# Performance work log

Measured on AMD Instinct MI355X. Metric: run time of the kernel, lower is better.

## Reference

```python
import jax, jax.numpy as jnp
import numpy as np

B, T, D, H = 512, 512, 128, 64


def _lstm(x, Wih, Whh, b):
    """Single-layer batch-first LSTM, PyTorch gate order (i, f, g, o).
    x: [B, T, Din]; Wih: [4Hc, Din]; Whh: [4Hc, Hc]; b: [4Hc] (= b_ih + b_hh).
    Returns (outputs [B, T, Hc], final_hidden [B, Hc]).
    """
    Hc = Whh.shape[1]
    Bn = x.shape[0]
    # Precompute input projections for all timesteps: [B, T, 4Hc]
    xp = jnp.einsum('bti,gi->btg', x, Wih) + b

    def step(carry, xt):
        h, c = carry
        g = xt + h @ Whh.T                      # [B, 4Hc]
        i = jax.nn.sigmoid(g[:, :Hc])
        f = jax.nn.sigmoid(g[:, Hc:2 * Hc])
        gg = jnp.tanh(g[:, 2 * Hc:3 * Hc])
        o = jax.nn.sigmoid(g[:, 3 * Hc:])
        c = f * c + i * gg
        h = o * jnp.tanh(c)
        return (h, c), h

    init = (jnp.zeros((Bn, Hc), x.dtype), jnp.zeros((Bn, Hc), x.dtype))
    (h_last, _), ys = jax.lax.scan(step, init, jnp.swapaxes(xp, 0, 1))
    return jnp.swapaxes(ys, 0, 1), h_last


def setup_inputs() -> dict:
    key = jax.random.key(0)
    ks = jax.random.split(key, 7)
    se = 1.0 / np.sqrt(H)   # PyTorch LSTM init scale (encoder, hidden=H)
    sd = 1.0 / np.sqrt(D)   # decoder, hidden=D
    return {
        'x': jax.random.normal(ks[0], (B, T, D), jnp.float32),
        'Wih_e': jax.random.uniform(ks[1], (4 * H, D), jnp.float32, -se, se),
        'Whh_e': jax.random.uniform(ks[2], (4 * H, H), jnp.float32, -se, se),
        'b_e': jax.random.uniform(ks[3], (4 * H,), jnp.float32, -se, se),
        'Wih_d': jax.random.uniform(ks[4], (4 * D, H), jnp.float32, -sd, sd),
        'Whh_d': jax.random.uniform(ks[5], (4 * D, D), jnp.float32, -sd, sd),
        'b_d': jax.random.uniform(ks[6], (4 * D,), jnp.float32, -sd, sd),
    }


def reference(x, Wih_e, Whh_e, b_e, Wih_d, Whh_d, b_d):
    # Encoder: take final hidden state [B, H]
    _, h = _lstm(x, Wih_e, Whh_e, b_e)
    # hidden.repeat(T,1,1).permute(1,0,2) -> tile across time: [B, T, H]
    hrep = jnp.broadcast_to(h[:, None, :], (h.shape[0], x.shape[1], h.shape[1]))
    # Decoder: full output sequence [B, T, D]
    reconstructed, _ = _lstm(hrep, Wih_d, Whh_d, b_d)
    return reconstructed
```

## Files before the change

kernel.cpp:

```cpp
#include <hip/hip_runtime.h>

#define TT 512

typedef float f32x4 __attribute__((ext_vector_type(4)));

template<int CTRL>
__device__ __forceinline__ float dpp_mov(float v) {
    return __int_as_float(__builtin_amdgcn_mov_dpp(__float_as_int(v), CTRL, 0xF, 0xF, true));
}
__device__ __forceinline__ float swz_xor4(float v) {
    return __int_as_float(__builtin_amdgcn_ds_swizzle(__float_as_int(v), 0x101F));
}

#define LOG2E 1.4426950408889634f
#define NEG2LOG2E -2.8853900817779268f

__device__ __forceinline__ float merge8(float* s) {
    s[0] += dpp_mov<0xB1>(s[4]);
    s[1] += dpp_mov<0xB1>(s[5]);
    s[2] += dpp_mov<0xB1>(s[6]);
    s[3] += dpp_mov<0xB1>(s[7]);
    s[0] += dpp_mov<0x4E>(s[2]);
    s[1] += dpp_mov<0x4E>(s[3]);
    return s[0] + swz_xor4(s[1]);
}

__global__ __launch_bounds__(1024, 4)
void dec_kernel(const float* __restrict__ h_enc,
                const float* __restrict__ Wih,
                const float* __restrict__ Whh,
                const float* __restrict__ bias,
                float* __restrict__ out)
{
    const int tid = threadIdx.x;
    const int gg  = tid >> 3;
    const int q   = tid & 7;
    const int q0 = q & 1, q1 = (q >> 1) & 1, q2 = (q >> 2) & 1;
    const int msk2 = (q0 << 1) | q1;
    const int b0  = blockIdx.x * 2;

    __shared__ __align__(16) float he[2][64];
    __shared__ __align__(16) float hb[2][2 * 160];

    if (tid < 128) he[tid >> 6][tid & 63] = h_enc[(size_t)(b0 + (tid >> 6)) * 64 + (tid & 63)];
    if (tid < 256) {
        int r = tid >> 7, j = tid & 127;
        hb[0][r * 160 + j + 4 * (j >> 4)] = 0.f;
    }

    f32x4 w[4][4];
    #pragma unroll
    for (int m = 0; m < 4; ++m) {
        const float* src = Whh + (size_t)((m ^ msk2) * 128 + gg) * 128 + 16 * q;
        #pragma unroll
        for (int c = 0; c < 4; ++c) w[m][c] = *(const f32x4*)(src + 4 * c);
    }

    const int t4own = 2 * q0 + q1;
    const float sA = (t4own == 2) ? 2.f : 1.f;
    const float sC = (t4own == 2) ? -1.f : 0.f;
    const float nsA = -LOG2E * sA;
    const bool writer = (q0 == 0) && (q1 == 0);
    const int rr  = q2;
    const int oA  = q2 * 160;
    const int oB  = (q2 ^ 1) * 160;
    const int kres = 20 * q;
    const int pwj = q2 * 160 + gg + 4 * (gg >> 4);

    __syncthreads();

    float xp;
    {
        const float* heA = he[q2] + 8 * q;
        const float* heB = he[q2 ^ 1] + 8 * q;
        f32x4 hA0 = *(const f32x4*)heA, hA1 = *(const f32x4*)(heA + 4);
        f32x4 hB0 = *(const f32x4*)heB, hB1 = *(const f32x4*)(heB + 4);
        float s[8];
        #pragma unroll
        for (int m = 0; m < 4; ++m) {
            const float* ws = Wih + (size_t)((m ^ msk2) * 128 + gg) * 64 + 8 * q;
            f32x4 w0 = *(const f32x4*)ws, w1 = *(const f32x4*)(ws + 4);
            float aA = 0.f, aB = 0.f;
            aA = fmaf(w0.x, hA0.x, aA); aA = fmaf(w0.y, hA0.y, aA);
            aA = fmaf(w0.z, hA0.z, aA); aA = fmaf(w0.w, hA0.w, aA);
            aA = fmaf(w1.x, hA1.x, aA); aA = fmaf(w1.y, hA1.y, aA);
            aA = fmaf(w1.z, hA1.z, aA); aA = fmaf(w1.w, hA1.w, aA);
            aB = fmaf(w0.x, hB0.x, aB); aB = fmaf(w0.y, hB0.y, aB);
            aB = fmaf(w0.z, hB0.z, aB); aB = fmaf(w0.w, hB0.w, aB);
            aB = fmaf(w1.x, hB1.x, aB); aB = fmaf(w1.y, hB1.y, aB);
            aB = fmaf(w1.z, hB1.z, aB); aB = fmaf(w1.w, hB1.w, aB);
            s[2 * m]     = aA;
            s[2 * m + 1] = aB;
        }
        xp = merge8(s) + bias[t4own * 128 + gg];
    }

    float c_state = 0.f;
    size_t optr = ((size_t)(b0 + rr) * TT) * 128 + gg;

#define DSTEP(CUR, NXT) {                                                      \
    const float* bAp = (CUR) + oA + kres;                                      \
    const float* bBp = (CUR) + oB + kres;                                      \
    f32x4 ch[4]; float s[8];                                                   \
    _Pragma("unroll") for (int c = 0; c < 4; ++c) ch[c] = *(const f32x4*)(bAp + 4 * c); \
    _Pragma("unroll") for (int m = 0; m < 4; ++m) { float a = 0.f;             \
        _Pragma("unroll") for (int c = 0; c < 4; ++c) {                        \
            a = fmaf(w[m][c].x, ch[c].x, a); a = fmaf(w[m][c].y, ch[c].y, a);  \
            a = fmaf(w[m][c].z, ch[c].z, a); a = fmaf(w[m][c].w, ch[c].w, a); }\
        s[2 * m] = a; }                                                        \
    _Pragma("unroll") for (int c = 0; c < 4; ++c) ch[c] = *(const f32x4*)(bBp + 4 * c); \
    _Pragma("unroll") for (int m = 0; m < 4; ++m) { float a = 0.f;             \
        _Pragma("unroll") for (int c = 0; c < 4; ++c) {                        \
            a = fmaf(w[m][c].x, ch[c].x, a); a = fmaf(w[m][c].y, ch[c].y, a);  \
            a = fmaf(w[m][c].z, ch[c].z, a); a = fmaf(w[m][c].w, ch[c].w, a); }\
        s[2 * m + 1] = a; }                                                    \
    float z = merge8(s) + xp;                                                  \
    float ez = __builtin_amdgcn_exp2f(z * nsA);                                \
    float v  = fmaf(__builtin_amdgcn_rcpf(1.0f + ez), sA, sC);                 \
    float vi = dpp_mov<0x00>(v); float vg = dpp_mov<0x55>(v);                  \
    float vf = dpp_mov<0xAA>(v); float vo = dpp_mov<0xFF>(v);                  \
    c_state = fmaf(vf, c_state, vi * vg);                                      \
    float e2 = __builtin_amdgcn_exp2f(c_state * NEG2LOG2E);                    \
    float hv = vo * fmaf(__builtin_amdgcn_rcpf(1.f + e2), 2.f, -1.f);          \
    if (writer) { (NXT)[pwj] = hv; out[optr] = hv; }                           \
    optr += 128;                                                               \
    __syncthreads(); }

    #pragma unroll 1
    for (int t = 0; t < TT; t += 2) {
        DSTEP(hb[0], hb[1]);
        DSTEP(hb[1], hb[0]);
    }
#undef DSTEP
}

__global__ __launch_bounds__(512, 2)
void enc_kernel(const float* __restrict__ x,
                const float* __restrict__ Wih,
                const float* __restrict__ Whh,
                const float* __restrict__ bias,
                float* __restrict__ h_out)
{
    const int tid = threadIdx.x;
    const int gg  = tid >> 3;
    const int q   = tid & 7;
    const int q0 = q & 1, q1 = (q >> 1) & 1, q2 = (q >> 2) & 1;
    const int msk2 = (q0 << 1) | q1;
    const int b0  = blockIdx.x * 2;

    __shared__ __align__(16) float xh[2][2 * 224];

    f32x4 w[4][6];
    #pragma unroll
    for (int m = 0; m < 4; ++m) {
        int row = (m ^ msk2) * 64 + gg;
        #pragma unroll
        for (int c = 0; c < 6; ++c) {
            int k0 = 24 * q + 4 * c;
            const float* src = (k0 < 128) ? (Wih + (size_t)row * 128 + k0)
                                          : (Whh + (size_t)row * 64 + (k0 - 128));
            w[m][c] = *(const f32x4*)src;
        }
    }

    const int t4own = 2 * q0 + q1;
    const float sA = (t4own == 2) ? 2.f : 1.f;
    const float sC = (t4own == 2) ? -1.f : 0.f;
    const float nsA = -LOG2E * sA;
    const bool writer = (q0 == 0) && (q1 == 0);
    const int rr  = q2;
    const int oA  = q2 * 224;
    const int oB  = (q2 ^ 1) * 224;
    const int kres = 28 * q;
    const int hj  = 128 + gg;
    const int pwj = q2 * 224 + hj + 4 * (hj / 24);
    const float xpc = bias[t4own * 64 + gg];

    const bool stager = (tid < 64);
    const int sr = (tid >> 5) & 1, sc = tid & 31;
    const int psl = sr * 224 + 4 * sc + 4 * ((4 * sc) / 24);
    const float* xbase = x + ((size_t)(b0 + sr) * TT) * 128 + 4 * sc;

    if (stager) *(f32x4*)(&xh[0][psl]) = *(const f32x4*)xbase;
    if (tid < 128) {
        int r = tid >> 6, j = 128 + (tid & 63);
        xh[0][r * 224 + j + 4 * (j / 24)] = 0.f;
    }

    float c_state = 0.f;
    float h_last = 0.f;
    __syncthreads();

#define ESTEP(CUR, NXT, T) {                                                   \
    f32x4 xnext;                                                               \
    if (stager) { int tl = (T) + 1 < TT ? (T) + 1 : TT - 1;                    \
        xnext = *(const f32x4*)(xbase + (size_t)tl * 128); }                   \
    const float* bAp = (CUR) + oA + kres;                                      \
    const float* bBp = (CUR) + oB + kres;                                      \
    f32x4 ch[6]; float s[8];                                                   \
    _Pragma("unroll") for (int c = 0; c < 6; ++c) ch[c] = *(const f32x4*)(bAp + 4 * c); \
    _Pragma("unroll") for (int m = 0; m < 4; ++m) { float a = 0.f;             \
        _Pragma("unroll") for (int c = 0; c < 6; ++c) {                        \
            a = fmaf(w[m][c].x, ch[c].x, a); a = fmaf(w[m][c].y, ch[c].y, a);  \
            a = fmaf(w[m][c].z, ch[c].z, a); a = fmaf(w[m][c].w, ch[c].w, a); }\
        s[2 * m] = a; }                                                        \
    _Pragma("unroll") for (int c = 0; c < 6; ++c) ch[c] = *(const f32x4*)(bBp + 4 * c); \
    _Pragma("unroll") for (int m = 0; m < 4; ++m) { float a = 0.f;             \
        _Pragma("unroll") for (int c = 0; c < 6; ++c) {                        \
            a = fmaf(w[m][c].x, ch[c].x, a); a = fmaf(w[m][c].y, ch[c].y, a);  \
            a = fmaf(w[m][c].z, ch[c].z, a); a = fmaf(w[m][c].w, ch[c].w, a); }\
        s[2 * m + 1] = a; }                                                    \
    float z = merge8(s) + xpc;                                                 \
    float ez = __builtin_amdgcn_exp2f(z * nsA);                                \
    float v  = fmaf(__builtin_amdgcn_rcpf(1.0f + ez), sA, sC);                 \
    float vi = dpp_mov<0x00>(v); float vg = dpp_mov<0x55>(v);                  \
    float vf = dpp_mov<0xAA>(v); float vo = dpp_mov<0xFF>(v);                  \
    c_state = fmaf(vf, c_state, vi * vg);                                      \
    float e2 = __builtin_amdgcn_exp2f(c_state * NEG2LOG2E);                    \
    float hv = vo * fmaf(__builtin_amdgcn_rcpf(1.f + e2), 2.f, -1.f);          \
    h_last = hv;                                                               \
    if (writer) (NXT)[pwj] = hv;                                               \
    if (stager) *(f32x4*)((NXT) + psl) = xnext;                                \
    __syncthreads(); }

    #pragma unroll 1
    for (int t = 0; t < TT; t += 2) {
        ESTEP(xh[0], xh[1], t);
        ESTEP(xh[1], xh[0], t + 1);
    }
#undef ESTEP

    if (writer) h_out[(size_t)(b0 + rr) * 64 + gg] = h_last;
}

extern "C" void kernel_launch(void* const* d_in, const int* in_sizes, int n_in,
                              void* d_out, int out_size, void* d_ws, size_t ws_size,
                              hipStream_t stream) {
    const float* x     = (const float*)d_in[0];
    const float* Wih_e = (const float*)d_in[1];
    const float* Whh_e = (const float*)d_in[2];
    const float* b_e   = (const float*)d_in[3];
    const float* Wih_d = (const float*)d_in[4];
    const float* Whh_d = (const float*)d_in[5];
    const float* b_d   = (const float*)d_in[6];
    float* out   = (float*)d_out;
    float* h_enc = (float*)d_ws;

    enc_kernel<<<dim3(256), dim3(512), 0, stream>>>(x, Wih_e, Whh_e, b_e, h_enc);
    dec_kernel<<<dim3(256), dim3(1024), 0, stream>>>(h_enc, Wih_d, Whh_d, b_d, out);
}
```

Baseline: 1.016 ms.

## Halve decoder block to 512 threads with 4 lanes per gate row

The decoder now uses 4 lanes per hidden unit instead of 8, each lane holding 32 columns of Whh in registers (128 floats), and each thread computes both batch rows per step. The block shrinks from 1024 to 512 threads, which cuts the cross-lane reduction from three stages to two and makes the per-step barrier cheaper. In exchange each thread does twice the FMAs per step and register pressure rises sharply, so occupancy drops or spills may appear. The shared hidden-state buffer is re-padded to a 148-float stride.

```diff
diff --git a/kernel.cpp b/kernel.cpp
--- a/kernel.cpp
+++ b/kernel.cpp
@@ -25,7 +25,7 @@
     return s[0] + swz_xor4(s[1]);
 }
 
-__global__ __launch_bounds__(1024, 4)
+__global__ __launch_bounds__(512, 2)
 void dec_kernel(const float* __restrict__ h_enc,
                 const float* __restrict__ Wih,
                 const float* __restrict__ Whh,
@@ -33,97 +33,122 @@
                 float* __restrict__ out)
 {
     const int tid = threadIdx.x;
-    const int gg  = tid >> 3;
-    const int q   = tid & 7;
-    const int q0 = q & 1, q1 = (q >> 1) & 1, q2 = (q >> 2) & 1;
+    const int gg  = tid >> 2;
+    const int q   = tid & 3;
+    const int q0 = q & 1, q1 = (q >> 1) & 1;
     const int msk2 = (q0 << 1) | q1;
     const int b0  = blockIdx.x * 2;
 
     __shared__ __align__(16) float he[2][64];
-    __shared__ __align__(16) float hb[2][2 * 160];
+    __shared__ __align__(16) float hb[2][2 * 148];
 
     if (tid < 128) he[tid >> 6][tid & 63] = h_enc[(size_t)(b0 + (tid >> 6)) * 64 + (tid & 63)];
-    if (tid < 256) {
-        int r = tid >> 7, j = tid & 127;
-        hb[0][r * 160 + j + 4 * (j >> 4)] = 0.f;
-    }
-
-    f32x4 w[4][4];
+    if (tid < 296) hb[0][tid] = 0.f;
+
+    f32x4 w[4][8];
     #pragma unroll
     for (int m = 0; m < 4; ++m) {
-        const float* src = Whh + (size_t)((m ^ msk2) * 128 + gg) * 128 + 16 * q;
+        const float* src = Whh + (size_t)((m ^ msk2) * 128 + gg) * 128 + 32 * q;
         #pragma unroll
-        for (int c = 0; c < 4; ++c) w[m][c] = *(const f32x4*)(src + 4 * c);
-    }
-
-    const int t4own = 2 * q0 + q1;
-    const float sA = (t4own == 2) ? 2.f : 1.f;
-    const float sC = (t4own == 2) ? -1.f : 0.f;
+        for (int c = 0; c < 8; ++c) w[m][c] = *(const f32x4*)(src + 4 * c);
+    }
+
+    const float sA = (msk2 == 2) ? 2.f : 1.f;
+    const float sC = (msk2 == 2) ? -1.f : 0.f;
     const float nsA = -LOG2E * sA;
-    const bool writer = (q0 == 0) && (q1 == 0);
-    const int rr  = q2;
-    const int oA  = q2 * 160;
-    const int oB  = (q2 ^ 1) * 160;
-    const int kres = 20 * q;
-    const int pwj = q2 * 160 + gg + 4 * (gg >> 4);
+    const bool writer = (q == 0);
+    const int kres = 36 * q;
+    const int pj   = (gg >> 5) * 36 + (gg & 31);
 
     __syncthreads();
 
-    float xp;
+    float xpA, xpB;
     {
-        const float* heA = he[q2] + 8 * q;
-        const float* heB = he[q2 ^ 1] + 8 * q;
-        f32x4 hA0 = *(const f32x4*)heA, hA1 = *(const f32x4*)(heA + 4);
-        f32x4 hB0 = *(const f32x4*)heB, hB1 = *(const f32x4*)(heB + 4);
+        const float* h0 = he[0] + 16 * q;
+        const float* h1 = he[1] + 16 * q;
+        f32x4 a0 = *(const f32x4*)h0, a1 = *(const f32x4*)(h0 + 4);
+        f32x4 a2 = *(const f32x4*)(h0 + 8), a3 = *(const f32x4*)(h0 + 12);
+        f32x4 b0v = *(const f32x4*)h1, b1v = *(const f32x4*)(h1 + 4);
+        f32x4 b2v = *(const f32x4*)(h1 + 8), b3v = *(const f32x4*)(h1 + 12);
         float s[8];
         #pragma unroll
         for (int m = 0; m < 4; ++m) {
-            const float* ws = Wih + (size_t)((m ^ msk2) * 128 + gg) * 64 + 8 * q;
-            f32x4 w0 = *(const f32x4*)ws, w1 = *(const f32x4*)(ws + 4);
+            const float* ws = Wih + (size_t)((m ^ msk2) * 128 + gg) * 64 + 16 * q;
+            f32x4 w0 = *(const f32x4*)ws,       w1 = *(const f32x4*)(ws + 4);
+            f32x4 w2 = *(const f32x4*)(ws + 8), w3 = *(const f32x4*)(ws + 12);
             float aA = 0.f, aB = 0.f;
-            aA = fmaf(w0.x, hA0.x, aA); aA = fmaf(w0.y, hA0.y, aA);
-            aA = fmaf(w0.z, hA0.z, aA); aA = fmaf(w0.w, hA0.w, aA);
-            aA = fmaf(w1.x, hA1.x, aA); aA = fmaf(w1.y, hA1.y, aA);
-            aA = fmaf(w1.z, hA1.z, aA); aA = fmaf(w1.w, hA1.w, aA);
-            aB = fmaf(w0.x, hB0.x, aB); aB = fmaf(w0.y, hB0.y, aB);
-            aB = fmaf(w0.z, hB0.z, aB); aB = fmaf(w0.w, hB0.w, aB);
-            aB = fmaf(w1.x, hB1.x, aB); aB = fmaf(w1.y, hB1.y, aB);
-            aB = fmaf(w1.z, hB1.z, aB); aB = fmaf(w1.w, hB1.w, aB);
+            aA = fmaf(w0.x, a0.x, aA); aA = fmaf(w0.y, a0.y, aA);
+            aA = fmaf(w0.z, a0.z, aA); aA = fmaf(w0.w, a0.w, aA);
+            aA = fmaf(w1.x, a1.x, aA); aA = fmaf(w1.y, a1.y, aA);
+            aA = fmaf(w1.z, a1.z, aA); aA = fmaf(w1.w, a1.w, aA);
+            aA = fmaf(w2.x, a2.x, aA); aA = fmaf(w2.y, a2.y, aA);
+            aA = fmaf(w2.z, a2.z, aA); aA = fmaf(w2.w, a2.w, aA);
+            aA = fmaf(w3.x, a3.x, aA); aA = fmaf(w3.y, a3.y, aA);
+            aA = fmaf(w3.z, a3.z, aA); aA = fmaf(w3.w, a3.w, aA);
+            aB = fmaf(w0.x, b0v.x, aB); aB = fmaf(w0.y, b0v.y, aB);
+            aB = fmaf(w0.z, b0v.z, aB); aB = fmaf(w0.w, b0v.w, aB);
+            aB = fmaf(w1.x, b1v.x, aB); aB = fmaf(w1.y, b1v.y, aB);
+            aB = fmaf(w1.z, b1v.z, aB); aB = fmaf(w1.w, b1v.w, aB);
+            aB = fmaf(w2.x, b2v.x, aB); aB = fmaf(w2.y, b2v.y, aB);
+            aB = fmaf(w2.z, b2v.z, aB); aB = fmaf(w2.w, b2v.w, aB);
+            aB = fmaf(w3.x, b3v.x, aB); aB = fmaf(w3.y, b3v.y, aB);
+            aB = fmaf(w3.z, b3v.z, aB); aB = fmaf(w3.w, b3v.w, aB);
             s[2 * m]     = aA;
             s[2 * m + 1] = aB;
         }
-        xp = merge8(s) + bias[t4own * 128 + gg];
-    }
-
-    float c_state = 0.f;
-    size_t optr = ((size_t)(b0 + rr) * TT) * 128 + gg;
+        s[0] += dpp_mov<0xB1>(s[4]); s[1] += dpp_mov<0xB1>(s[5]);
+        s[2] += dpp_mov<0xB1>(s[6]); s[3] += dpp_mov<0xB1>(s[7]);
+        s[0] += dpp_mov<0x4E>(s[2]); s[1] += dpp_mov<0x4E>(s[3]);
+        const float bb = bias[msk2 * 128 + gg];
+        xpA = s[0] + bb;
+        xpB = s[1] + bb;
+    }
+
+    float cA = 0.f, cB = 0.f;
+    size_t optrA = ((size_t)(b0 + 0) * TT) * 128 + gg;
+    size_t optrB = ((size_t)(b0 + 1) * TT) * 128 + gg;
 
 #define DSTEP(CUR, NXT) {                                                      \
-    const float* bAp = (CUR) + oA + kres;                                      \
-    const float* bBp = (CUR) + oB + kres;                                      \
-    f32x4 ch[4]; float s[8];                                                   \
-    _Pragma("unroll") for (int c = 0; c < 4; ++c) ch[c] = *(const f32x4*)(bAp + 4 * c); \
-    _Pragma("unroll") for (int m = 0; m < 4; ++m) { float a = 0.f;             \
-        _Pragma("unroll") for (int c = 0; c < 4; ++c) {                        \
-            a = fmaf(w[m][c].x, ch[c].x, a); a = fmaf(w[m][c].y, ch[c].y, a);  \
-            a = fmaf(w[m][c].z, ch[c].z, a); a = fmaf(w[m][c].w, ch[c].w, a); }\
+    const float* p0 = (CUR) + kres;                                            \
+    const float* p1 = (CUR) + 148 + kres;                                      \
+    f32x4 ch0[8], ch1[8];                                                      \
+    _Pragma("unroll") for (int c = 0; c < 8; ++c) ch0[c] = *(const f32x4*)(p0 + 4 * c); \
+    _Pragma("unroll") for (int c = 0; c < 8; ++c) ch1[c] = *(const f32x4*)(p1 + 4 * c); \
+    float s[8];                                                                \
+    _Pragma("unroll") for (int m = 0; m < 4; ++m) { float a = 0.f;             \
+        _Pragma("unroll") for (int c = 0; c < 8; ++c) {                        \
+            a = fmaf(w[m][c].x, ch0[c].x, a); a = fmaf(w[m][c].y, ch0[c].y, a);\
+            a = fmaf(w[m][c].z, ch0[c].z, a); a = fmaf(w[m][c].w, ch0[c].w, a);}\
         s[2 * m] = a; }                                                        \
-    _Pragma("unroll") for (int c = 0; c < 4; ++c) ch[c] = *(const f32x4*)(bBp + 4 * c); \
-    _Pragma("unroll") for (int m = 0; m < 4; ++m) { float a = 0.f;             \
-        _Pragma("unroll") for (int c = 0; c < 4; ++c) {                        \
-            a = fmaf(w[m][c].x, ch[c].x, a); a = fmaf(w[m][c].y, ch[c].y, a);  \
-            a = fmaf(w[m][c].z, ch[c].z, a); a = fmaf(w[m][c].w, ch[c].w, a); }\
+    _Pragma("unroll") for (int m = 0; m < 4; ++m) { float a = 0.f;             \
+        _Pragma("unroll") for (int c = 0; c < 8; ++c) {                        \
+            a = fmaf(w[m][c].x, ch1[c].x, a); a = fmaf(w[m][c].y, ch1[c].y, a);\
+            a = fmaf(w[m][c].z, ch1[c].z, a); a = fmaf(w[m][c].w, ch1[c].w, a);}\
         s[2 * m + 1] = a; }                                                    \
-    float z = merge8(s) + xp;                                                  \
-    float ez = __builtin_amdgcn_exp2f(z * nsA);                                \
-    float v  = fmaf(__builtin_amdgcn_rcpf(1.0f + ez), sA, sC);                 \
-    float vi = dpp_mov<0x00>(v); float vg = dpp_mov<0x55>(v);                  \
-    float vf = dpp_mov<0xAA>(v); float vo = dpp_mov<0xFF>(v);                  \
-    c_state = fmaf(vf, c_state, vi * vg);                                      \
-    float e2 = __builtin_amdgcn_exp2f(c_state * NEG2LOG2E);                    \
-    float hv = vo * fmaf(__builtin_amdgcn_rcpf(1.f + e2), 2.f, -1.f);          \
-    if (writer) { (NXT)[pwj] = hv; out[optr] = hv; }                           \
-    optr += 128;                                                               \
+    s[0] += dpp_mov<0xB1>(s[4]); s[1] += dpp_mov<0xB1>(s[5]);                  \
+    s[2] += dpp_mov<0xB1>(s[6]); s[3] += dpp_mov<0xB1>(s[7]);                  \
+    s[0] += dpp_mov<0x4E>(s[2]); s[1] += dpp_mov<0x4E>(s[3]);                  \
+    float zA = s[0] + xpA;                                                     \
+    float zB = s[1] + xpB;                                                     \
+    float ezA = __builtin_amdgcn_exp2f(zA * nsA);                              \
+    float vA  = fmaf(__builtin_amdgcn_rcpf(1.0f + ezA), sA, sC);               \
+    float ezB = __builtin_amdgcn_exp2f(zB * nsA);                              \
+    float vB  = fmaf(__builtin_amdgcn_rcpf(1.0f + ezB), sA, sC);               \
+    float viA = dpp_mov<0x00>(vA); float vgA = dpp_mov<0x55>(vA);              \
+    float vfA = dpp_mov<0xAA>(vA); float voA = dpp_mov<0xFF>(vA);              \
+    float viB = dpp_mov<0x00>(vB); float vgB = dpp_mov<0x55>(vB);              \
+    float vfB = dpp_mov<0xAA>(vB); float voB = dpp_mov<0xFF>(vB);              \
+    cA = fmaf(vfA, cA, viA * vgA);                                             \
+    cB = fmaf(vfB, cB, viB * vgB);                                             \
+    float e2A = __builtin_amdgcn_exp2f(cA * NEG2LOG2E);                        \
+    float hvA = voA * fmaf(__builtin_amdgcn_rcpf(1.f + e2A), 2.f, -1.f);       \
+    float e2B = __builtin_amdgcn_exp2f(cB * NEG2LOG2E);                        \
+    float hvB = voB * fmaf(__builtin_amdgcn_rcpf(1.f + e2B), 2.f, -1.f);       \
+    if (writer) {                                                              \
+        (NXT)[pj] = hvA; (NXT)[148 + pj] = hvB;                                \
+        out[optrA] = hvA; out[optrB] = hvB;                                    \
+    }                                                                          \
+    optrA += 128; optrB += 128;                                                \
     __syncthreads(); }
 
     #pragma unroll 1
@@ -247,5 +272,5 @@
     float* h_enc = (float*)d_ws;
 
     enc_kernel<<<dim3(256), dim3(512), 0, stream>>>(x, Wih_e, Whh_e, b_e, h_enc);
-    dec_kernel<<<dim3(256), dim3(1024), 0, stream>>>(h_enc, Wih_d, Whh_d, b_d, out);
-}
+    dec_kernel<<<dim3(256), dim3(512), 0, stream>>>(h_enc, Wih_d, Whh_d, b_d, out);
+}
```

Result: no change. 1.035 ms (+1.9%).

## Split encoder to one batch row per block and raise occupancy bound

Applied to the files above, without the earlier changes.

The encoder kernel now gives each block a single batch row instead of two, doubling the grid to 512 blocks. Each thread's per-step dot product shrinks from two rows to one, and the cross-lane reduction is shortened to match. The aim is to cut the serial per-timestep latency of the recurrent loop. Launch bounds rise to 4 blocks per CU, which caps VGPRs. That risks spilling the 96-register weight cache.

```diff
diff --git a/kernel.cpp b/kernel.cpp
--- a/kernel.cpp
+++ b/kernel.cpp
@@ -134,7 +134,7 @@
 #undef DSTEP
 }
 
-__global__ __launch_bounds__(512, 2)
+__global__ __launch_bounds__(512, 4)
 void enc_kernel(const float* __restrict__ x,
                 const float* __restrict__ Wih,
                 const float* __restrict__ Whh,
@@ -144,47 +144,42 @@
     const int tid = threadIdx.x;
     const int gg  = tid >> 3;
     const int q   = tid & 7;
-    const int q0 = q & 1, q1 = (q >> 1) & 1, q2 = (q >> 2) & 1;
+    const int q0 = q & 1, q1 = (q >> 1) & 1;
     const int msk2 = (q0 << 1) | q1;
-    const int b0  = blockIdx.x * 2;
-
-    __shared__ __align__(16) float xh[2][2 * 224];
+    const int row = blockIdx.x;
+
+    __shared__ __align__(16) float xh[2][224];
 
     f32x4 w[4][6];
     #pragma unroll
     for (int m = 0; m < 4; ++m) {
-        int row = (m ^ msk2) * 64 + gg;
+        int wr = (m ^ msk2) * 64 + gg;
         #pragma unroll
         for (int c = 0; c < 6; ++c) {
             int k0 = 24 * q + 4 * c;
-            const float* src = (k0 < 128) ? (Wih + (size_t)row * 128 + k0)
-                                          : (Whh + (size_t)row * 64 + (k0 - 128));
+            const float* src = (k0 < 128) ? (Wih + (size_t)wr * 128 + k0)
+                                          : (Whh + (size_t)wr * 64 + (k0 - 128));
             w[m][c] = *(const f32x4*)src;
         }
     }
 
-    const int t4own = 2 * q0 + q1;
-    const float sA = (t4own == 2) ? 2.f : 1.f;
-    const float sC = (t4own == 2) ? -1.f : 0.f;
+    const float sA = (msk2 == 2) ? 2.f : 1.f;
+    const float sC = (msk2 == 2) ? -1.f : 0.f;
     const float nsA = -LOG2E * sA;
-    const bool writer = (q0 == 0) && (q1 == 0);
-    const int rr  = q2;
-    const int oA  = q2 * 224;
-    const int oB  = (q2 ^ 1) * 224;
+    const bool writer = (q == 0);
     const int kres = 28 * q;
     const int hj  = 128 + gg;
-    const int pwj = q2 * 224 + hj + 4 * (hj / 24);
-    const float xpc = bias[t4own * 64 + gg];
-
-    const bool stager = (tid < 64);
-    const int sr = (tid >> 5) & 1, sc = tid & 31;
-    const int psl = sr * 224 + 4 * sc + 4 * ((4 * sc) / 24);
-    const float* xbase = x + ((size_t)(b0 + sr) * TT) * 128 + 4 * sc;
+    const int pwj = hj + 4 * (hj / 24);
+    const float xpc = bias[msk2 * 64 + gg];
+
+    const bool stager = (tid < 32);
+    const int psl = 4 * tid + 4 * ((4 * tid) / 24);
+    const float* xbase = x + (size_t)row * TT * 128 + 4 * tid;
 
     if (stager) *(f32x4*)(&xh[0][psl]) = *(const f32x4*)xbase;
-    if (tid < 128) {
-        int r = tid >> 6, j = 128 + (tid & 63);
-        xh[0][r * 224 + j + 4 * (j / 24)] = 0.f;
+    if (tid < 64) {
+        int j = 128 + tid;
+        xh[0][j + 4 * (j / 24)] = 0.f;
     }
 
     float c_state = 0.f;
@@ -195,22 +190,36 @@
     f32x4 xnext;                                                               \
     if (stager) { int tl = (T) + 1 < TT ? (T) + 1 : TT - 1;                    \
         xnext = *(const f32x4*)(xbase + (size_t)tl * 128); }                   \
-    const float* bAp = (CUR) + oA + kres;                                      \
-    const float* bBp = (CUR) + oB + kres;                                      \
-    f32x4 ch[6]; float s[8];                                                   \
-    _Pragma("unroll") for (int c = 0; c < 6; ++c) ch[c] = *(const f32x4*)(bAp + 4 * c); \
-    _Pragma("unroll") for (int m = 0; m < 4; ++m) { float a = 0.f;             \
-        _Pragma("unroll") for (int c = 0; c < 6; ++c) {                        \
-            a = fmaf(w[m][c].x, ch[c].x, a); a = fmaf(w[m][c].y, ch[c].y, a);  \
-            a = fmaf(w[m][c].z, ch[c].z, a); a = fmaf(w[m][c].w, ch[c].w, a); }\
-        s[2 * m] = a; }                                                        \
-    _Pragma("unroll") for (int c = 0; c < 6; ++c) ch[c] = *(const f32x4*)(bBp + 4 * c); \
-    _Pragma("unroll") for (int m = 0; m < 4; ++m) { float a = 0.f;             \
-        _Pragma("unroll") for (int c = 0; c < 6; ++c) {                        \
-            a = fmaf(w[m][c].x, ch[c].x, a); a = fmaf(w[m][c].y, ch[c].y, a);  \
-            a = fmaf(w[m][c].z, ch[c].z, a); a = fmaf(w[m][c].w, ch[c].w, a); }\
-        s[2 * m + 1] = a; }                                                    \
-    float z = merge8(s) + xpc;                                                 \
+    const float* bp = (CUR) + kres;                                            \
+    float s[4];                                                                \
+    {              \
+        f32x4 c0 = *(const f32x4*)(bp), c1 = *(const f32x4*)(bp + 4),          \
+              c2 = *(const f32x4*)(bp + 8);                                    \
+        _Pragma("unroll") for (int m = 0; m < 4; ++m) { float a = 0.f;         \
+            a = fmaf(w[m][0].x, c0.x, a); a = fmaf(w[m][0].y, c0.y, a);        \
+            a = fmaf(w[m][0].z, c0.z, a); a = fmaf(w[m][0].w, c0.w, a);        \
+            a = fmaf(w[m][1].x, c1.x, a); a = fmaf(w[m][1].y, c1.y, a);        \
+            a = fmaf(w[m][1].z, c1.z, a); a = fmaf(w[m][1].w, c1.w, a);        \
+            a = fmaf(w[m][2].x, c2.x, a); a = fmaf(w[m][2].y, c2.y, a);        \
+            a = fmaf(w[m][2].z, c2.z, a); a = fmaf(w[m][2].w, c2.w, a);        \
+            s[m] = a; }                                                        \
+    }                                                                          \
+    {                                             \
+        f32x4 c0 = *(const f32x4*)(bp + 12), c1 = *(const f32x4*)(bp + 16),    \
+              c2 = *(const f32x4*)(bp + 20);                                   \
+        _Pragma("unroll") for (int m = 0; m < 4; ++m) { float a = s[m];        \
+            a = fmaf(w[m][3].x, c0.x, a); a = fmaf(w[m][3].y, c0.y, a);        \
+            a = fmaf(w[m][3].z, c0.z, a); a = fmaf(w[m][3].w, c0.w, a);        \
+            a = fmaf(w[m][4].x, c1.x, a); a = fmaf(w[m][4].y, c1.y, a);        \
+            a = fmaf(w[m][4].z, c1.z, a); a = fmaf(w[m][4].w, c1.w, a);        \
+            a = fmaf(w[m][5].x, c2.x, a); a = fmaf(w[m][5].y, c2.y, a);        \
+            a = fmaf(w[m][5].z, c2.z, a); a = fmaf(w[m][5].w, c2.w, a);        \
+            s[m] = a; }                                                        \
+    }                                                                          \
+       \
+    s[0] += dpp_mov<0xB1>(s[2]); s[1] += dpp_mov<0xB1>(s[3]);                  \
+    s[0] += dpp_mov<0x4E>(s[1]);                                               \
+    float z = s[0] + swz_xor4(s[0]) + xpc;                                     \
     float ez = __builtin_amdgcn_exp2f(z * nsA);                                \
     float v  = fmaf(__builtin_amdgcn_rcpf(1.0f + ez), sA, sC);                 \
     float vi = dpp_mov<0x00>(v); float vg = dpp_mov<0x55>(v);                  \
@@ -230,7 +239,7 @@
     }
 #undef ESTEP
 
-    if (writer) h_out[(size_t)(b0 + rr) * 64 + gg] = h_last;
+    if (writer) h_out[(size_t)row * 64 + gg] = h_last;
 }
 
 extern "C" void kernel_launch(void* const* d_in, const int* in_sizes, int n_in,
@@ -246,6 +255,6 @@
     float* out   = (float*)d_out;
     float* h_enc = (float*)d_ws;
 
-    enc_kernel<<<dim3(256), dim3(512), 0, stream>>>(x, Wih_e, Whh_e, b_e, h_enc);
+    enc_kernel<<<dim3(512), dim3(512), 0, stream>>>(x, Wih_e, Whh_e, b_e, h_enc);
     dec_kernel<<<dim3(256), dim3(1024), 0, stream>>>(h_enc, Wih_d, Whh_d, b_d, out);
 }
```

Result: faster. 988.8 us (-2.7%).
